# Kernel optimization log

Hardware: AMD Instinct MI355X
Metric: run time of the kernel (lower is better)

## Reference

```python
import jax, jax.numpy as jnp
import numpy as np

B = 512          # batch of visual features
VF_D = 4096      # visual feature dim (VGG fc7)
HID_D = 2048     # hidden dim
EMB_D = 300      # order-embedding / label-vector dim
N_LABELS = 2000  # number of GT label vectors


def setup_inputs() -> dict:
    key = jax.random.key(0)
    ks = jax.random.split(key, 4)
    vfs = jax.random.normal(ks[0], (B, VF_D), dtype=jnp.float32)
    W1 = jax.random.normal(ks[1], (VF_D, HID_D), dtype=jnp.float32) * (1.0 / np.sqrt(VF_D))
    b1 = jnp.zeros((HID_D,), dtype=jnp.float32)
    W2 = jax.random.normal(ks[2], (HID_D, EMB_D), dtype=jnp.float32) * (1.0 / np.sqrt(HID_D))
    b2 = jnp.zeros((EMB_D,), dtype=jnp.float32)
    gt_label_vecs = jax.random.normal(ks[3], (N_LABELS, EMB_D), dtype=jnp.float32)
    return {"vfs": vfs, "W1": W1, "b1": b1, "W2": W2, "b2": b2,
            "gt_label_vecs": gt_label_vecs}


def reference(vfs, W1, b1, W2, b2, gt_label_vecs):
    # hidden_layer: ReLU -> (Dropout, identity at eval) -> Linear
    vf_hidden = jnp.dot(jax.nn.relu(vfs), W1) + b1            # [B, HID_D]
    # embedding_layer: ReLU -> Linear
    vf_emb = jnp.dot(jax.nn.relu(vf_hidden), W2) + b2         # [B, EMB_D]
    # order_sim(hypers=gt_label_vecs, hypos=vf_emb):
    #   score = -|| clamp(hypo - hyper, min=0) ||^2, batched over all pairs
    diff = jax.nn.relu(vf_emb[:, None, :] - gt_label_vecs[None, :, :])  # [B, N, D]
    score_stack = -jnp.sum(diff * diff, axis=-1)              # [B, N_LABELS]
    return score_stack, vf_emb
```

## Files before the change

kernel.cpp:

```cpp
#include <hip/hip_runtime.h>

#define B_SZ   512
#define VFD    4096
#define HIDD   2048
#define EMBD   300
#define NLAB   2000

#define G1_SPLIT 4
#define G2_SPLIT 8

typedef __attribute__((ext_vector_type(8))) short short8x;
typedef __attribute__((ext_vector_type(4))) float f32x4;
typedef __attribute__((ext_vector_type(8))) unsigned short ushort8;
typedef __attribute__((ext_vector_type(2))) _Float16 h2;

typedef const __attribute__((address_space(1))) unsigned int* gas_t;
typedef __attribute__((address_space(3))) unsigned int* las_t;

__device__ inline unsigned short f2bf(float x) {
    unsigned u = __float_as_uint(x);
    u += 0x7FFF + ((u >> 16) & 1);
    return (unsigned short)(u >> 16);
}

__device__ inline unsigned short f2hneg(float x) {
    _Float16 h = (_Float16)(-x);
    return __builtin_bit_cast(unsigned short, h);
}

__device__ inline h2 pkrtz(float a, float b) {
    return __builtin_bit_cast(h2, __builtin_amdgcn_cvt_pkrtz(a, b));
}

__global__ __launch_bounds__(256) void prep_kernel(
    const float* __restrict__ vfs, unsigned short* __restrict__ Xb,
    const float* __restrict__ W1, unsigned short* __restrict__ W1T,
    const float* __restrict__ W2, unsigned short* __restrict__ W2T,
    const float* __restrict__ G,  unsigned short* __restrict__ Gh,
    const float* __restrict__ b2, float* __restrict__ E)
{
    __shared__ unsigned int Lds[64][34];
    const int tid = threadIdx.x;
    const int blk = blockIdx.x;

    if (blk < 1024) {
        const int i = (blk * 256 + tid) * 8;
        float4 a = *(const float4*)&vfs[i];
        float4 b = *(const float4*)&vfs[i + 4];
        ushort8 o;
        o[0] = f2bf(fmaxf(a.x, 0.f)); o[1] = f2bf(fmaxf(a.y, 0.f));
        o[2] = f2bf(fmaxf(a.z, 0.f)); o[3] = f2bf(fmaxf(a.w, 0.f));
        o[4] = f2bf(fmaxf(b.x, 0.f)); o[5] = f2bf(fmaxf(b.y, 0.f));
        o[6] = f2bf(fmaxf(b.z, 0.f)); o[7] = f2bf(fmaxf(b.w, 0.f));
        *(ushort8*)&Xb[i] = o;
        return;
    }
    if (blk >= 3525) {
        const int i = ((blk - 3525) * 256 + tid) * 4;
        const int n = i % EMBD;
        float4 bv = *(const float4*)&b2[n];
        *(float4*)&E[i] = bv;
        return;
    }
    if (blk >= 3232) {
        const int i = ((blk - 3232) * 256 + tid) * 8;
        if (i + 8 <= NLAB * EMBD) {
            float4 a = *(const float4*)&G[i];
            float4 b = *(const float4*)&G[i + 4];
            ushort8 o;
            o[0] = f2hneg(a.x); o[1] = f2hneg(a.y);
            o[2] = f2hneg(a.z); o[3] = f2hneg(a.w);
            o[4] = f2hneg(b.x); o[5] = f2hneg(b.y);
            o[6] = f2hneg(b.z); o[7] = f2hneg(b.w);
            *(ushort8*)&Gh[i] = o;
        }
        return;
    }

    const float* in; unsigned short* out; int N, ldK, bx, by;
    if (blk < 3072) {
        const int b = blk - 1024;
        in = W1; out = W1T; N = HIDD; ldK = VFD; bx = b & 31; by = b >> 5;
    } else {
        const int b = blk - 3072;
        in = W2; out = W2T; N = EMBD; ldK = HIDD; bx = b % 5; by = b / 5;
    }
    const int n0 = bx * 64, k0 = by * 64;

    #pragma unroll
    for (int i = 0; i < 2; ++i) {
        const int s = tid + 256 * i;
        const int kp = s >> 4, nq = s & 15;
        const int n = n0 + nq * 4;
        float4 v0 = {0.f,0.f,0.f,0.f}, v1 = {0.f,0.f,0.f,0.f};
        if (n < N) {
            v0 = *(const float4*)&in[(size_t)(k0 + 2 * kp)     * N + n];
            v1 = *(const float4*)&in[(size_t)(k0 + 2 * kp + 1) * N + n];
        }
        Lds[nq*4+0][kp] = (unsigned)f2bf(v0.x) | ((unsigned)f2bf(v1.x) << 16);
        Lds[nq*4+1][kp] = (unsigned)f2bf(v0.y) | ((unsigned)f2bf(v1.y) << 16);
        Lds[nq*4+2][kp] = (unsigned)f2bf(v0.z) | ((unsigned)f2bf(v1.z) << 16);
        Lds[nq*4+3][kp] = (unsigned)f2bf(v0.w) | ((unsigned)f2bf(v1.w) << 16);
    }
    __syncthreads();

    #pragma unroll
    for (int i = 0; i < 2; ++i) {
        const int c = tid + 256 * i;
        const int n = c >> 3, oct = c & 7;
        uint2 lo = *(uint2*)&Lds[n][oct * 4];
        uint2 hi = *(uint2*)&Lds[n][oct * 4 + 2];
        uint4 v = make_uint4(lo.x, lo.y, hi.x, hi.y);
        *(uint4*)&out[(size_t)(n0 + n) * ldK + k0 + oct * 8] = v;
    }
}

__global__ __launch_bounds__(256) void gemm1_kernel(
    const unsigned short* __restrict__ A,
    const unsigned short* __restrict__ Bt,
    unsigned short* __restrict__ Cpart)
{
    __shared__ unsigned short As[2][4096];
    __shared__ unsigned short Bs[2][8192];

    const int tid = threadIdx.x;
    const int m0 = blockIdx.y * 64, n0 = blockIdx.x * 128;
    const int kbase = blockIdx.z * (VFD / G1_SPLIT);

    const unsigned short* ga = A + (size_t)(m0 + (tid & 63)) * VFD + kbase + (tid >> 6) * 8;
    const unsigned short* gb = Bt + (size_t)(n0 + (tid & 127)) * VFD + kbase + (tid >> 7) * 8;

    const int lane = tid & 63;
    const int wave = tid >> 6;
    const int wm = (wave & 1) * 32;
    const int wn = (wave >> 1) * 64;
    const int q = lane >> 4, l15 = lane & 15;

    f32x4 acc[2][4];
    #pragma unroll
    for (int r = 0; r < 2; ++r)
        #pragma unroll
        for (int c = 0; c < 4; ++c) acc[r][c] = (f32x4){0.f,0.f,0.f,0.f};

    #pragma unroll
    for (int i = 0; i < 2; ++i)
        __builtin_amdgcn_global_load_lds((gas_t)(const void*)(ga + i * 32),
                                         (las_t)(void*)&As[0][(tid + 256 * i) * 8], 16, 0, 0);
    #pragma unroll
    for (int i = 0; i < 4; ++i)
        __builtin_amdgcn_global_load_lds((gas_t)(const void*)(gb + i * 16),
                                         (las_t)(void*)&Bs[0][(tid + 256 * i) * 8], 16, 0, 0);

    const int iters = (VFD / G1_SPLIT) / 64;
    for (int t = 0; t < iters; ++t) {
        const int cur = t & 1, nxt = cur ^ 1;
        __syncthreads();

        if (t + 1 < iters) {
            const int ko = (t + 1) * 64;
            #pragma unroll
            for (int i = 0; i < 2; ++i)
                __builtin_amdgcn_global_load_lds((gas_t)(const void*)(ga + ko + i * 32),
                                                 (las_t)(void*)&As[nxt][(tid + 256 * i) * 8], 16, 0, 0);
            #pragma unroll
            for (int i = 0; i < 4; ++i)
                __builtin_amdgcn_global_load_lds((gas_t)(const void*)(gb + ko + i * 16),
                                                 (las_t)(void*)&Bs[nxt][(tid + 256 * i) * 8], 16, 0, 0);
        }

        #pragma unroll
        for (int kk = 0; kk < 2; ++kk) {
            const int oct = kk * 4 + q;
            short8x a0 = *(short8x*)&As[cur][(oct * 64 + wm +      l15) * 8];
            short8x a1 = *(short8x*)&As[cur][(oct * 64 + wm + 16 + l15) * 8];
            #pragma unroll
            for (int c = 0; c < 4; ++c) {
                short8x b = *(short8x*)&Bs[cur][(oct * 128 + wn + c * 16 + l15) * 8];
                acc[0][c] = __builtin_amdgcn_mfma_f32_16x16x32_bf16(a0, b, acc[0][c], 0, 0, 0);
                acc[1][c] = __builtin_amdgcn_mfma_f32_16x16x32_bf16(a1, b, acc[1][c], 0, 0, 0);
            }
        }
    }

    unsigned short* Cz = Cpart + (size_t)blockIdx.z * B_SZ * HIDD;
    #pragma unroll
    for (int r = 0; r < 2; ++r) {
        #pragma unroll
        for (int g = 0; g < 4; ++g) {
            const int rr = m0 + wm + r * 16 + q * 4 + g;
            #pragma unroll
            for (int c = 0; c < 4; ++c)
                Cz[(size_t)rr * HIDD + n0 + wn + c * 16 + l15] = f2bf(acc[r][c][g]);
        }
    }
}

__global__ __launch_bounds__(256) void gemm2_kernel(
    const unsigned short* __restrict__ A,
    const unsigned short* __restrict__ Bt,
    float* __restrict__ E)
{
    __shared__ unsigned short As[2][4096];
    __shared__ unsigned short Bs[2][4096];

    const int tid = threadIdx.x;
    const int m0 = blockIdx.y * 64, n0 = blockIdx.x * 64;
    const int kbase = blockIdx.z * (HIDD / G2_SPLIT);

    const unsigned short* ga = A  + (size_t)(m0 + (tid & 63)) * HIDD + kbase + (tid >> 6) * 8;
    const unsigned short* gb = Bt + (size_t)(n0 + (tid & 63)) * HIDD + kbase + (tid >> 6) * 8;

    const int lane = tid & 63;
    const int wave = tid >> 6;
    const int wm = (wave & 1) * 32;
    const int wn = (wave >> 1) * 32;
    const int q = lane >> 4, l15 = lane & 15;

    f32x4 acc00 = {0.f,0.f,0.f,0.f}, acc01 = {0.f,0.f,0.f,0.f};
    f32x4 acc10 = {0.f,0.f,0.f,0.f}, acc11 = {0.f,0.f,0.f,0.f};

    #pragma unroll
    for (int i = 0; i < 2; ++i) {
        __builtin_amdgcn_global_load_lds((gas_t)(const void*)(ga + i * 32),
                                         (las_t)(void*)&As[0][(tid + 256 * i) * 8], 16, 0, 0);
        __builtin_amdgcn_global_load_lds((gas_t)(const void*)(gb + i * 32),
                                         (las_t)(void*)&Bs[0][(tid + 256 * i) * 8], 16, 0, 0);
    }

    const int iters = (HIDD / G2_SPLIT) / 64;
    for (int t = 0; t < iters; ++t) {
        const int cur = t & 1, nxt = cur ^ 1;
        __syncthreads();

        if (t + 1 < iters) {
            const int ko = (t + 1) * 64;
            #pragma unroll
            for (int i = 0; i < 2; ++i) {
                __builtin_amdgcn_global_load_lds((gas_t)(const void*)(ga + ko + i * 32),
                                                 (las_t)(void*)&As[nxt][(tid + 256 * i) * 8], 16, 0, 0);
                __builtin_amdgcn_global_load_lds((gas_t)(const void*)(gb + ko + i * 32),
                                                 (las_t)(void*)&Bs[nxt][(tid + 256 * i) * 8], 16, 0, 0);
            }
        }

        #pragma unroll
        for (int kk = 0; kk < 2; ++kk) {
            const int oct = kk * 4 + q;
            short8x a0 = *(short8x*)&As[cur][(oct * 64 + wm +      l15) * 8];
            short8x a1 = *(short8x*)&As[cur][(oct * 64 + wm + 16 + l15) * 8];
            short8x b0 = *(short8x*)&Bs[cur][(oct * 64 + wn +      l15) * 8];
            short8x b1 = *(short8x*)&Bs[cur][(oct * 64 + wn + 16 + l15) * 8];
            acc00 = __builtin_amdgcn_mfma_f32_16x16x32_bf16(a0, b0, acc00, 0, 0, 0);
            acc01 = __builtin_amdgcn_mfma_f32_16x16x32_bf16(a0, b1, acc01, 0, 0, 0);
            acc10 = __builtin_amdgcn_mfma_f32_16x16x32_bf16(a1, b0, acc10, 0, 0, 0);
            acc11 = __builtin_amdgcn_mfma_f32_16x16x32_bf16(a1, b1, acc11, 0, 0, 0);
        }
    }

    #pragma unroll
    for (int r = 0; r < 4; ++r) {
        const int rr = m0 + wm + q * 4 + r;
        const int cc = n0 + wn + l15;
        if (cc < EMBD) {
            atomicAdd(&E[(size_t)rr * EMBD + cc],        acc00[r]);
            atomicAdd(&E[(size_t)(rr + 16) * EMBD + cc], acc10[r]);
        }
        if (cc + 16 < EMBD) {
            atomicAdd(&E[(size_t)rr * EMBD + cc + 16],        acc01[r]);
            atomicAdd(&E[(size_t)(rr + 16) * EMBD + cc + 16], acc11[r]);
        }
    }
}

__global__ __launch_bounds__(256) void reduce_h_kernel(
    const unsigned short* __restrict__ Hpart, const float* __restrict__ b1,
    unsigned short* __restrict__ Hb)
{
    const int i = (blockIdx.x * 256 + threadIdx.x) * 8;
    const int col = i & (HIDD - 1);
    float s[8];
    float4 ba = *(const float4*)&b1[col];
    float4 bb = *(const float4*)&b1[col + 4];
    s[0]=ba.x; s[1]=ba.y; s[2]=ba.z; s[3]=ba.w;
    s[4]=bb.x; s[5]=bb.y; s[6]=bb.z; s[7]=bb.w;
    #pragma unroll
    for (int z = 0; z < G1_SPLIT; ++z) {
        ushort8 p = *(const ushort8*)&Hpart[(size_t)z * B_SZ * HIDD + i];
        #pragma unroll
        for (int j = 0; j < 8; ++j)
            s[j] += __uint_as_float((unsigned)p[j] << 16);
    }
    ushort8 o;
    #pragma unroll
    for (int j = 0; j < 8; ++j) o[j] = f2bf(fmaxf(s[j], 0.f));
    *(ushort8*)&Hb[i] = o;
}

__global__ __launch_bounds__(256) void scores_kernel(
    const float* __restrict__ E,
    const unsigned short* __restrict__ Gh,
    float* __restrict__ scores)
{
    __shared__ unsigned short Gs[64][60];

    const int tid = threadIdx.x;
    const int tx = tid & 15, ty = tid >> 4;
    const int n0 = blockIdx.x * 64, b0 = blockIdx.y * 32;

    const h2 hz = {(_Float16)0.0f, (_Float16)0.0f};
    float acc[2][4] = {};

    for (int d0 = 0; d0 < EMBD; d0 += 60) {
        __syncthreads();
        #pragma unroll
        for (int i = 0; i < 4; ++i) {
            const int s = tid + 256 * i;
            if (s < 960) {
                const int row = s / 15, qd = (s - row * 15) * 4;
                const int n = n0 + row;
                uint2 v = make_uint2(0u, 0u);
                if (n < NLAB) v = *(const uint2*)&Gh[(size_t)n * EMBD + d0 + qd];
                *(uint2*)&Gs[row][qd] = v;
            }
        }
        __syncthreads();

        #pragma unroll
        for (int d = 0; d < 60; d += 4) {
            const int dd = d0 + d;
            h2 e0[2], e1[2];
            #pragma unroll
            for (int r = 0; r < 2; ++r) {
                float4 ev = *(const float4*)&E[(size_t)(b0 + ty * 2 + r) * EMBD + dd];
                e0[r] = pkrtz(ev.x, ev.y);
                e1[r] = pkrtz(ev.z, ev.w);
            }
            #pragma unroll
            for (int c = 0; c < 4; ++c) {
                uint2 gv = *(const uint2*)&Gs[tx + 16 * c][d];
                const h2 g0 = __builtin_bit_cast(h2, gv.x);
                const h2 g1 = __builtin_bit_cast(h2, gv.y);
                #pragma unroll
                for (int r = 0; r < 2; ++r) {
                    h2 s0 = e0[r] + g0;
                    h2 s1 = e1[r] + g1;
                    s0 = __builtin_elementwise_max(s0, hz);
                    s1 = __builtin_elementwise_max(s1, hz);
                    acc[r][c] = __builtin_amdgcn_fdot2(s0, s0, acc[r][c], false);
                    acc[r][c] = __builtin_amdgcn_fdot2(s1, s1, acc[r][c], false);
                }
            }
        }
    }

    #pragma unroll
    for (int r = 0; r < 2; ++r) {
        const int b = b0 + ty * 2 + r;
        #pragma unroll
        for (int c = 0; c < 4; ++c) {
            const int n = n0 + tx + 16 * c;
            if (n < NLAB) scores[(size_t)b * NLAB + n] = -acc[r][c];
        }
    }
}

extern "C" void kernel_launch(void* const* d_in, const int* in_sizes, int n_in,
                              void* d_out, int out_size, void* d_ws, size_t ws_size,
                              hipStream_t stream)
{
    const float* vfs = (const float*)d_in[0];
    const float* W1  = (const float*)d_in[1];
    const float* b1  = (const float*)d_in[2];
    const float* W2  = (const float*)d_in[3];
    const float* b2  = (const float*)d_in[4];
    const float* G   = (const float*)d_in[5];

    float* out    = (float*)d_out;
    float* scores = out;
    float* E      = out + (size_t)B_SZ * NLAB;

    char* ws = (char*)d_ws;
    unsigned short* Xb  = (unsigned short*)(ws);
    unsigned short* W1T = (unsigned short*)(ws + 4194304);
    unsigned short* W2T = (unsigned short*)(ws + 20971520);
    unsigned short* Hb  = (unsigned short*)(ws + 22282240);
    unsigned short* Hpart = (unsigned short*)(ws + 24379392);
    unsigned short* Gh  = (unsigned short*)(ws + 32768000);

    prep_kernel<<<3675, 256, 0, stream>>>(vfs, Xb, W1, W1T, W2, W2T, G, Gh, b2, E);

    gemm1_kernel<<<dim3(16, 8, G1_SPLIT), 256, 0, stream>>>(Xb, W1T, Hpart);
    reduce_h_kernel<<<512, 256, 0, stream>>>(Hpart, b1, Hb);

    gemm2_kernel<<<dim3(5, 8, G2_SPLIT), 256, 0, stream>>>(Hb, W2T, E);

    scores_kernel<<<dim3(32, 16), 256, 0, stream>>>(E, Gh, scores);
}
```

Before: 168.5 us.

## Replace gemm2 atomic split-K with partial buffers and a separate reduce kernel

Gemm2 now writes its split-K partial sums to a padded float workspace instead of using atomicAdd into E, and a new reduce kernel adds the partials plus the bias. The same kernel also writes an fp16 copy of E, which the scores kernel reads directly instead of loading fp32 and converting. The bias initialisation of E moves out of the prep kernel. This removes atomic contention and halves the E traffic in the scores kernel, at the cost of one extra kernel launch and extra workspace traffic.

```diff
diff --git a/kernel.cpp b/kernel.cpp
--- a/kernel.cpp
+++ b/kernel.cpp
@@ -5,6 +5,7 @@
 #define HIDD   2048
 #define EMBD   300
 #define NLAB   2000
+#define NPAD   320
 
 #define G1_SPLIT 4
 #define G2_SPLIT 8
@@ -28,16 +29,11 @@
     return __builtin_bit_cast(unsigned short, h);
 }
 
-__device__ inline h2 pkrtz(float a, float b) {
-    return __builtin_bit_cast(h2, __builtin_amdgcn_cvt_pkrtz(a, b));
-}
-
 __global__ __launch_bounds__(256) void prep_kernel(
     const float* __restrict__ vfs, unsigned short* __restrict__ Xb,
     const float* __restrict__ W1, unsigned short* __restrict__ W1T,
     const float* __restrict__ W2, unsigned short* __restrict__ W2T,
-    const float* __restrict__ G,  unsigned short* __restrict__ Gh,
-    const float* __restrict__ b2, float* __restrict__ E)
+    const float* __restrict__ G,  unsigned short* __restrict__ Gh)
 {
     __shared__ unsigned int Lds[64][34];
     const int tid = threadIdx.x;
@@ -55,13 +51,6 @@
         *(ushort8*)&Xb[i] = o;
         return;
     }
-    if (blk >= 3525) {
-        const int i = ((blk - 3525) * 256 + tid) * 4;
-        const int n = i % EMBD;
-        float4 bv = *(const float4*)&b2[n];
-        *(float4*)&E[i] = bv;
-        return;
-    }
     if (blk >= 3232) {
         const int i = ((blk - 3232) * 256 + tid) * 8;
         if (i + 8 <= NLAB * EMBD) {
@@ -198,7 +187,7 @@
 __global__ __launch_bounds__(256) void gemm2_kernel(
     const unsigned short* __restrict__ A,
     const unsigned short* __restrict__ Bt,
-    float* __restrict__ E)
+    float* __restrict__ Cpart)
 {
     __shared__ unsigned short As[2][4096];
     __shared__ unsigned short Bs[2][4096];
@@ -257,18 +246,15 @@
         }
     }
 
+    float* Cz = Cpart + (size_t)blockIdx.z * B_SZ * NPAD;
     #pragma unroll
     for (int r = 0; r < 4; ++r) {
         const int rr = m0 + wm + q * 4 + r;
         const int cc = n0 + wn + l15;
-        if (cc < EMBD) {
-            atomicAdd(&E[(size_t)rr * EMBD + cc],        acc00[r]);
-            atomicAdd(&E[(size_t)(rr + 16) * EMBD + cc], acc10[r]);
-        }
-        if (cc + 16 < EMBD) {
-            atomicAdd(&E[(size_t)rr * EMBD + cc + 16],        acc01[r]);
-            atomicAdd(&E[(size_t)(rr + 16) * EMBD + cc + 16], acc11[r]);
-        }
+        Cz[(size_t)rr * NPAD + cc]             = acc00[r];
+        Cz[(size_t)rr * NPAD + cc + 16]        = acc01[r];
+        Cz[(size_t)(rr + 16) * NPAD + cc]      = acc10[r];
+        Cz[(size_t)(rr + 16) * NPAD + cc + 16] = acc11[r];
     }
 }
 
@@ -296,8 +282,23 @@
     *(ushort8*)&Hb[i] = o;
 }
 
+__global__ __launch_bounds__(256) void reduce_e_kernel(
+    const float* __restrict__ Epart, const float* __restrict__ b2,
+    float* __restrict__ E, unsigned short* __restrict__ Eh)
+{
+    const int gid = blockIdx.x * 256 + threadIdx.x;
+    if (gid >= B_SZ * EMBD) return;
+    const int m = gid / EMBD, n = gid - m * EMBD;
+    float v = b2[n];
+    #pragma unroll
+    for (int z = 0; z < G2_SPLIT; ++z)
+        v += Epart[(size_t)z * B_SZ * NPAD + m * NPAD + n];
+    E[gid] = v;
+    Eh[gid] = __builtin_bit_cast(unsigned short, (_Float16)v);
+}
+
 __global__ __launch_bounds__(256) void scores_kernel(
-    const float* __restrict__ E,
+    const unsigned short* __restrict__ Eh,
     const unsigned short* __restrict__ Gh,
     float* __restrict__ scores)
 {
@@ -331,9 +332,9 @@
             h2 e0[2], e1[2];
             #pragma unroll
             for (int r = 0; r < 2; ++r) {
-                float4 ev = *(const float4*)&E[(size_t)(b0 + ty * 2 + r) * EMBD + dd];
-                e0[r] = pkrtz(ev.x, ev.y);
-                e1[r] = pkrtz(ev.z, ev.w);
+                uint2 ev = *(const uint2*)&Eh[(size_t)(b0 + ty * 2 + r) * EMBD + dd];
+                e0[r] = __builtin_bit_cast(h2, ev.x);
+                e1[r] = __builtin_bit_cast(h2, ev.y);
             }
             #pragma unroll
             for (int c = 0; c < 4; ++c) {
@@ -386,13 +387,16 @@
     unsigned short* Hb  = (unsigned short*)(ws + 22282240);
     unsigned short* Hpart = (unsigned short*)(ws + 24379392);
     unsigned short* Gh  = (unsigned short*)(ws + 32768000);
-
-    prep_kernel<<<3675, 256, 0, stream>>>(vfs, Xb, W1, W1T, W2, W2T, G, Gh, b2, E);
+    float*          Epart = (float*)(ws + 33968128);
+    unsigned short* Eh  = (unsigned short*)(ws + 39211008);
+
+    prep_kernel<<<3525, 256, 0, stream>>>(vfs, Xb, W1, W1T, W2, W2T, G, Gh);
 
     gemm1_kernel<<<dim3(16, 8, G1_SPLIT), 256, 0, stream>>>(Xb, W1T, Hpart);
     reduce_h_kernel<<<512, 256, 0, stream>>>(Hpart, b1, Hb);
 
-    gemm2_kernel<<<dim3(5, 8, G2_SPLIT), 256, 0, stream>>>(Hb, W2T, E);
-
-    scores_kernel<<<dim3(32, 16), 256, 0, stream>>>(E, Gh, scores);
-}
+    gemm2_kernel<<<dim3(5, 8, G2_SPLIT), 256, 0, stream>>>(Hb, W2T, Epart);
+    reduce_e_kernel<<<600, 256, 0, stream>>>(Epart, b2, E, Eh);
+
+    scores_kernel<<<dim3(32, 16), 256, 0, stream>>>(Eh, Gh, scores);
+}
```

Result: faster. 162.8 us (-3.4%).
